# Optimization experiments

Measured on AMD Instinct MI355X. Metric: run time of the kernel, lower is better.

## Reference

```python
import jax, jax.numpy as jnp
import numpy as np
from jax.scipy.special import digamma, polygamma

N_ITERS = 100
TOL = 1e-3


def setup_inputs() -> dict:
    key = jax.random.key(0)
    x = jax.random.normal(key, (2_000_000, 10), dtype=jnp.float32)
    return {"x": x}


def reference(x):
    # x: [n, C] logits -> Dirichlet MLE over softmax probabilities
    p = jax.nn.softmax(x, axis=-1)            # [n, C]
    n = p.shape[0]
    m1 = p.mean(0)                            # [C] E[p]
    m2 = (p ** 2).mean(0)                     # [C] E[p^2]
    # method-of-moments initialization (as in the torch module)
    a0 = m1 * ((m1 - m2) / (m2 - m1 ** 2)).mean(-1)
    # loop-invariant sufficient statistic
    log_p_avg = jnp.log(p).mean(0)            # [C]

    def cond(carry):
        a, k, diff = carry
        return jnp.logical_and(k < N_ITERS, diff >= TOL)

    def body(carry):
        a, k, _ = carry
        g = (digamma(a.sum(-1)) - digamma(a) + log_p_avg) * n
        q = -n * polygamma(1, a)
        z = n * polygamma(1, a.sum(-1))
        q_inv = 1.0 / q
        b = (g * q_inv).sum(-1) / (1.0 / z + q_inv.sum(-1))
        a_new = a - (g - b) / q               # Newton step with rank-1 Hessian inverse
        diff = jnp.abs(a_new - a).sum()       # L1 norm, matches torch.norm(.,1)
        return (a_new, k + 1, diff)

    a, _, _ = jax.lax.while_loop(
        cond, body, (a0, jnp.int32(0), jnp.float32(jnp.inf))
    )
    return a.astype(jnp.float32)
```

## Files before the change

### kernel.cpp

```cpp
#include <hip/hip_runtime.h>
#include <math.h>

#define C 10
#define BLOCK 256
#define NBLOCKS 1024
#define TILE_ROWS 512
#define TILE_ELEMS (TILE_ROWS * C)
#define NSTATS (3 * C)


__device__ __forceinline__ void accum_row(const float* __restrict__ row,
                                          float* __restrict__ s1,
                                          float* __restrict__ s2,
                                          float* __restrict__ sl) {
  float v[C];
#pragma unroll
  for (int c = 0; c < C; c++) v[c] = row[c];
  float mx = v[0];
#pragma unroll
  for (int c = 1; c < C; c++) mx = fmaxf(mx, v[c]);
  float e[C], se = 0.f;
#pragma unroll
  for (int c = 0; c < C; c++) { v[c] -= mx; e[c] = __expf(v[c]); se += e[c]; }
  float inv = 1.0f / se;
  float lse = __logf(se);
#pragma unroll
  for (int c = 0; c < C; c++) {
    float p = e[c] * inv;
    s1[c] += p;
    s2[c] = fmaf(p, p, s2[c]);
    sl[c] += v[c] - lse;
  }
}

__global__ __launch_bounds__(BLOCK) void dir_stats_kernel(
    const float* __restrict__ x, float* __restrict__ partials,
    int nrows, int ntiles, int tailStart, int nblocks) {
  __shared__ float tile[TILE_ELEMS];
  const int tid = threadIdx.x;

  float s1[C], s2[C], sl[C];
#pragma unroll
  for (int c = 0; c < C; c++) { s1[c] = 0.f; s2[c] = 0.f; sl[c] = 0.f; }

  for (int t = blockIdx.x; t < ntiles; t += nblocks) {
    const float4* __restrict__ src = (const float4*)(x + (size_t)t * TILE_ELEMS);
    float4* dst = (float4*)tile;
#pragma unroll
    for (int i = 0; i < TILE_ELEMS / 4 / BLOCK; i++)
      dst[tid + i * BLOCK] = src[tid + i * BLOCK];
    __syncthreads();

#pragma unroll
    for (int r = 0; r < TILE_ROWS / BLOCK; r++)
      accum_row(tile + (size_t)(r * BLOCK + tid) * C, s1, s2, sl);
    __syncthreads();
  }

  if (blockIdx.x == nblocks - 1) {
    for (int rr = tailStart + tid; rr < nrows; rr += BLOCK)
      accum_row(x + (size_t)rr * C, s1, s2, sl);
  }

  const int lane = tid & 63;
  const int wave = tid >> 6;
  __shared__ float red[4][NSTATS];
#pragma unroll
  for (int c = 0; c < C; c++) {
    float v1 = s1[c], v2 = s2[c], v3 = sl[c];
#pragma unroll
    for (int off = 32; off >= 1; off >>= 1) {
      v1 += __shfl_down(v1, off);
      v2 += __shfl_down(v2, off);
      v3 += __shfl_down(v3, off);
    }
    if (lane == 0) {
      red[wave][c] = v1;
      red[wave][C + c] = v2;
      red[wave][2 * C + c] = v3;
    }
  }
  __syncthreads();
  if (tid < NSTATS) {
    float tot = red[0][tid] + red[1][tid] + red[2][tid] + red[3][tid];
    partials[(size_t)tid * nblocks + blockIdx.x] = tot;
  }
}


__device__ __forceinline__ void digtri(double x, double& dg, double& tg) {
  double rd = 0.0, rt = 0.0;
#pragma unroll 1
  for (int i = 0; i < 64 && x < 6.0; i++) {
    double inv = 1.0 / x;
    rd -= inv;
    rt += inv * inv;
    x += 1.0;
  }
  double xi = 1.0 / x, f = xi * xi;
  dg = log(x) - 0.5 * xi
     - f * (1.0 / 12 - f * (1.0 / 120 - f * (1.0 / 252 - f * (1.0 / 240 - f * (1.0 / 132)))))
     + rd;
  tg = rt + xi + 0.5 * f
     + f * xi * (1.0 / 6 - f * (1.0 / 30 - f * (1.0 / 42 - f * (1.0 / 30))));
}

__device__ __forceinline__ double wsum16(double v) {
#pragma unroll
  for (int off = 1; off < 16; off <<= 1) v += __shfl_xor(v, off);
  return v;
}

__global__ __launch_bounds__(1024) void dir_newton_kernel(
    const float* __restrict__ partials, float* __restrict__ out,
    int nparts, double nrows) {
  __shared__ double tot[NSTATS];
  const int tid = threadIdx.x;

  {
    const int j = tid >> 5;
    const int k = tid & 31;
    double s = 0.0;
    if (j < NSTATS) {
      const float* __restrict__ base = partials + (size_t)j * nparts;
#pragma unroll 8
      for (int b = k; b < nparts; b += 32)
        s += (double)base[b];
    }
#pragma unroll
    for (int off = 16; off >= 1; off >>= 1) s += __shfl_xor(s, off);
    if (j < NSTATS && k == 0) tot[j] = s;
  }
  __syncthreads();

  if (tid < 16) {
    const int c = tid;
    const bool act = (c < C);
    const double n = nrows;
    double m1 = 0.0, m2 = 0.0, lpa = 0.0;
    if (act) {
      m1 = tot[c] / n;
      m2 = tot[C + c] / n;
      lpa = tot[2 * C + c] / n;
    }
    double ratio = act ? (m1 - m2) / (m2 - m1 * m1) : 0.0;
    double rmean = wsum16(ratio) / (double)C;
    double a = act ? m1 * rmean : 0.0;

    double diff = 1e30;
    for (int k = 0; k < 100 && diff >= 1e-3; k++) {
      double S = wsum16(a);
      double dgS, tgS;
      digtri(S, dgS, tgS);
      double dga = 0.0, tga = 1.0;
      if (act) digtri(a, dga, tga);
      double g = act ? (dgS - dga + lpa) * n : 0.0;
      double qinv = act ? (-1.0) / (n * tga) : 0.0;
      double z = n * tgS;
      double num = wsum16(g * qinv);
      double den = 1.0 / z + wsum16(qinv);
      double b = num / den;
      double anew = act ? a - (g - b) * qinv : 0.0;
      diff = wsum16(act ? fabs(anew - a) : 0.0);
      a = anew;
    }
    if (act) out[c] = (float)a;
  }
}


extern "C" void kernel_launch(void* const* d_in, const int* in_sizes, int n_in,
                              void* d_out, int out_size, void* d_ws, size_t ws_size,
                              hipStream_t stream) {
  const float* x = (const float*)d_in[0];
  const int total = in_sizes[0];
  const int nrows = total / C;
  const int ntiles = nrows / TILE_ROWS;
  const int tailStart = ntiles * TILE_ROWS;

  int grid = NBLOCKS;
  size_t need = (size_t)NSTATS * grid * sizeof(float);
  if (need > ws_size) {
    grid = (int)(ws_size / (NSTATS * sizeof(float)));
    if (grid < 1) grid = 1;
  }

  float* partials = (float*)d_ws;
  dir_stats_kernel<<<grid, BLOCK, 0, stream>>>(x, partials, nrows, ntiles, tailStart, grid);
  dir_newton_kernel<<<1, 1024, 0, stream>>>(partials, (float*)d_out, grid, (double)nrows);
}
```

Measured before the change: 128.3 us.

## Double stats grid and use fixed-shift branchless digamma/trigamma in Newton loop

Doubles the number of stats blocks so the streaming pass has more parallelism. The Newton solver now replaces the data-dependent recurrence loop with a fixed eight-term shift, evaluated without branches. Lane 10 computes digamma/trigamma of the sum while lanes 0-9 compute per-class values, and the sum result is broadcast with a shuffle, so the two calls run in parallel instead of back to back. The fixed shift loses accuracy for very small arguments, and doubling the grid doubles the partials that the second kernel has to reduce.

```diff
diff --git a/kernel.cpp b/kernel.cpp
--- a/kernel.cpp
+++ b/kernel.cpp
@@ -3,7 +3,7 @@
 
 #define C 10
 #define BLOCK 256
-#define NBLOCKS 1024
+#define NBLOCKS 2048
 #define TILE_ROWS 512
 #define TILE_ELEMS (TILE_ROWS * C)
 #define NSTATS (3 * C)
@@ -50,7 +50,6 @@
     for (int i = 0; i < TILE_ELEMS / 4 / BLOCK; i++)
       dst[tid + i * BLOCK] = src[tid + i * BLOCK];
     __syncthreads();
-
 #pragma unroll
     for (int r = 0; r < TILE_ROWS / BLOCK; r++)
       accum_row(tile + (size_t)(r * BLOCK + tid) * C, s1, s2, sl);
@@ -88,21 +87,21 @@
 }
 
 
-__device__ __forceinline__ void digtri(double x, double& dg, double& tg) {
-  double rd = 0.0, rt = 0.0;
-#pragma unroll 1
-  for (int i = 0; i < 64 && x < 6.0; i++) {
-    double inv = 1.0 / x;
-    rd -= inv;
-    rt += inv * inv;
-    x += 1.0;
-  }
-  double xi = 1.0 / x, f = xi * xi;
-  dg = log(x) - 0.5 * xi
+__device__ __forceinline__ void digtri8(double x, double& dg, double& tg) {
+  double i0 = 1.0 / x,         i1 = 1.0 / (x + 1.0);
+  double i2 = 1.0 / (x + 2.0), i3 = 1.0 / (x + 3.0);
+  double i4 = 1.0 / (x + 4.0), i5 = 1.0 / (x + 5.0);
+  double i6 = 1.0 / (x + 6.0), i7 = 1.0 / (x + 7.0);
+  double rd = (i0 + i1) + (i2 + i3) + ((i4 + i5) + (i6 + i7));
+  double rt = (i0 * i0 + i1 * i1) + (i2 * i2 + i3 * i3) +
+              ((i4 * i4 + i5 * i5) + (i6 * i6 + i7 * i7));
+  double y = x + 8.0;
+  double yi = 1.0 / y, f = yi * yi;
+  dg = log(y) - 0.5 * yi
      - f * (1.0 / 12 - f * (1.0 / 120 - f * (1.0 / 252 - f * (1.0 / 240 - f * (1.0 / 132)))))
-     + rd;
-  tg = rt + xi + 0.5 * f
-     + f * xi * (1.0 / 6 - f * (1.0 / 30 - f * (1.0 / 42 - f * (1.0 / 30))));
+     - rd;
+  tg = rt + yi + 0.5 * f
+     + f * yi * (1.0 / 6 - f * (1.0 / 30 - f * (1.0 / 42 - f * (1.0 / 30))));
 }
 
 __device__ __forceinline__ double wsum16(double v) {
@@ -150,18 +149,18 @@
     double diff = 1e30;
     for (int k = 0; k < 100 && diff >= 1e-3; k++) {
       double S = wsum16(a);
-      double dgS, tgS;
-      digtri(S, dgS, tgS);
-      double dga = 0.0, tga = 1.0;
-      if (act) digtri(a, dga, tga);
-      double g = act ? (dgS - dga + lpa) * n : 0.0;
-      double qinv = act ? (-1.0) / (n * tga) : 0.0;
+      double dgl, tgl;
+      digtri8(act ? a : S, dgl, tgl);
+      double dgS = __shfl(dgl, 10);
+      double tgS = __shfl(tgl, 10);
+      double g = act ? (dgS - dgl + lpa) * n : 0.0;
+      double qinv = act ? (-1.0) / (n * tgl) : 0.0;
       double z = n * tgS;
       double num = wsum16(g * qinv);
       double den = 1.0 / z + wsum16(qinv);
       double b = num / den;
       double anew = act ? a - (g - b) * qinv : 0.0;
-      diff = wsum16(act ? fabs(anew - a) : 0.0);
+      diff = wsum16(fabs(anew - a));
       a = anew;
     }
     if (act) out[c] = (float)a;
```

Result: no change. 126.3 us (-1.5%).
